# Optimization experiments

Measured on AMD Instinct MI355X. Metric: run time of the kernel, lower is better.

## Reference

```python
import jax, jax.numpy as jnp
import numpy as np
import math

IN_FEATURES = 8192
OUT_FEATURES = 8192
IN_MODES = (32, 16, 16)   # balanced power-of-two split of 8192 over order 3
OUT_MODES = (32, 16, 16)
RANKS = (1, 4, 4, 1)
TOKENS = 128


def setup_inputs() -> dict:
    key = jax.random.key(0)
    k_in, k0, k1, k2, kb = jax.random.split(key, 5)
    inputs = jax.random.normal(k_in, (TOKENS, IN_FEATURES), dtype=jnp.float32)
    # cores: (left_rank, out_mode, in_mode, right_rank), init N(0, 0.02)
    core0 = 0.02 * jax.random.normal(k0, (RANKS[0], OUT_MODES[0], IN_MODES[0], RANKS[1]), dtype=jnp.float32)
    core1 = 0.02 * jax.random.normal(k1, (RANKS[1], OUT_MODES[1], IN_MODES[1], RANKS[2]), dtype=jnp.float32)
    core2 = 0.02 * jax.random.normal(k2, (RANKS[2], OUT_MODES[2], IN_MODES[2], RANKS[3]), dtype=jnp.float32)
    bound = 1.0 / math.sqrt(IN_FEATURES)
    bias = jax.random.uniform(kb, (OUT_FEATURES,), minval=-bound, maxval=bound, dtype=jnp.float32)
    return {"inputs": inputs, "core0": core0, "core1": core1, "core2": core2, "bias": bias}


def _dense_weight(core0, core1, core2):
    # chain contraction over TT ranks
    t = jnp.tensordot(core0, core1, axes=([-1], [0]))  # (1, o0, i0, o1, i1, r2)
    t = jnp.tensordot(t, core2, axes=([-1], [0]))      # (1, o0, i0, o1, i1, o2, i2, 1)
    t = jnp.squeeze(t, axis=(0, -1))                    # (o0, i0, o1, i1, o2, i2)
    # out modes first, then in modes (matches torch permute [0,2,4,1,3,5])
    t = jnp.transpose(t, (0, 2, 4, 1, 3, 5))
    w = t.reshape(math.prod(OUT_MODES), math.prod(IN_MODES))
    return w[:OUT_FEATURES, :IN_FEATURES]


def reference(inputs, core0, core1, core2, bias):
    weight = _dense_weight(core0, core1, core2)  # [out, in]
    return inputs @ weight.T + bias
```

## Files before the change

kernel.cpp:

```cpp
#include <hip/hip_runtime.h>

__global__ __launch_bounds__(256, 4) void tt_k12(
    const float* __restrict__ x, const float* __restrict__ c1,
    const float* __restrict__ c2, const float* __restrict__ c0,
    float* __restrict__ y2, float* __restrict__ c0t)
{
    __shared__ float xs[64 * 20];
    __shared__ float c2s[64 * 20];
    __shared__ float y1s[64 * 68];
    const int tid = threadIdx.x;
    const int b = blockIdx.x;
    const int t = b >> 3, i0q = b & 7;

    if (b < 16) {
        int idx = (b << 8) | tid;
        c0t[idx] = c0[(idx & 31) * 128 + (idx >> 5)];
    }

    {
        float4 v = reinterpret_cast<const float4*>(x + t * 8192 + i0q * 1024)[tid];
        *reinterpret_cast<float4*>(&xs[(tid >> 2) * 20 + ((tid & 3) << 2)]) = v;
    }
#pragma unroll
    for (int m = 0; m < 4; ++m) {
        int q = (m << 8) | tid;
        float4 v = reinterpret_cast<const float4*>(c2)[q];
        *reinterpret_cast<float4*>(&c2s[(q >> 2) * 20 + ((q & 3) << 2)]) = v;
    }
    __syncthreads();

    {
        const int i0loc = tid >> 6;
        const int o2 = (tid >> 2) & 15;
        const int i1q = tid & 3;
        float cw[4][16];
#pragma unroll
        for (int r2 = 0; r2 < 4; ++r2)
#pragma unroll
            for (int m = 0; m < 4; ++m) {
                float4 v = *reinterpret_cast<const float4*>(
                    &c2s[((r2 << 4) | o2) * 20 + (m << 2)]);
                cw[r2][4*m+0] = v.x; cw[r2][4*m+1] = v.y;
                cw[r2][4*m+2] = v.z; cw[r2][4*m+3] = v.w;
            }
#pragma unroll
        for (int d = 0; d < 4; ++d) {
            int i1 = (i1q << 2) | d;
            float xv[16];
#pragma unroll
            for (int m = 0; m < 4; ++m) {
                float4 v = *reinterpret_cast<const float4*>(
                    &xs[((i0loc << 4) | i1) * 20 + (m << 2)]);
                xv[4*m+0] = v.x; xv[4*m+1] = v.y; xv[4*m+2] = v.z; xv[4*m+3] = v.w;
            }
            float s[4];
#pragma unroll
            for (int r2 = 0; r2 < 4; ++r2) {
                float a = 0.f;
#pragma unroll
                for (int i2 = 0; i2 < 16; ++i2) a += xv[i2] * cw[r2][i2];
                s[r2] = a;
            }
            *reinterpret_cast<float4*>(&y1s[((i0loc << 4) | o2) * 68 + (i1 << 2)]) =
                make_float4(s[0], s[1], s[2], s[3]);
        }
    }
    __syncthreads();

    const int lane = tid & 63;
    const int w = __builtin_amdgcn_readfirstlane(tid >> 6);
    float acc[16];
#pragma unroll
    for (int r = 0; r < 16; ++r) acc[r] = 0.f;
    const float* yrow = &y1s[lane * 68];
    const float4* c14 = reinterpret_cast<const float4*>(c1);
#pragma unroll 2
    for (int jq = 0; jq < 16; ++jq) {
        float4 yv = *reinterpret_cast<const float4*>(yrow + (jq << 2));
#pragma unroll
        for (int o1 = 0; o1 < 16; ++o1) {
            float4 cv = c14[(((w << 4) | o1) << 4) | jq];
            acc[o1] += yv.x*cv.x + yv.y*cv.y + yv.z*cv.z + yv.w*cv.w;
        }
    }
    const int k = (((i0q << 2) | (lane >> 4)) << 2) | w;
    float* outp = y2 + (((t << 7) | k) << 8) + (lane & 15);
#pragma unroll
    for (int o1 = 0; o1 < 16; ++o1) outp[o1 << 4] = acc[o1];
}

__global__ __launch_bounds__(256, 2) void tt_k3(
    const float* __restrict__ y2, const float* __restrict__ c0t,
    const float* __restrict__ bias, float* __restrict__ out)
{
    __shared__ float po[3][32][64];
    const int tid = threadIdx.x;
    const int lane = tid & 63;
    const int kh = __builtin_amdgcn_readfirstlane(tid >> 6);
    const int b = blockIdx.x;
    const int t = b >> 2;
    const int c = ((b & 3) << 6) | lane;
    float acc[32];
#pragma unroll
    for (int m = 0; m < 32; ++m) acc[m] = 0.f;
    const float* yp = y2 + (t << 15) + c;
    const float4* c04 = reinterpret_cast<const float4*>(c0t);
#pragma unroll 4
    for (int kk = 0; kk < 32; ++kk) {
        int k = (kh << 5) | kk;
        float v = yp[k << 8];
#pragma unroll
        for (int m = 0; m < 8; ++m) {
            float4 cv = c04[(k << 3) | m];
            acc[4*m+0] += cv.x * v;
            acc[4*m+1] += cv.y * v;
            acc[4*m+2] += cv.z * v;
            acc[4*m+3] += cv.w * v;
        }
    }
    if (kh != 0) {
#pragma unroll
        for (int m = 0; m < 32; ++m) po[kh-1][m][lane] = acc[m];
    }
    __syncthreads();
    if (kh == 0) {
#pragma unroll
        for (int m = 0; m < 32; ++m) {
            float s = acc[m] + po[0][m][lane] + po[1][m][lane] + po[2][m][lane]
                    + bias[(m << 8) | c];
            out[(t << 13) | (m << 8) | c] = s;
        }
    }
}

extern "C" void kernel_launch(void* const* d_in, const int* in_sizes, int n_in,
                              void* d_out, int out_size, void* d_ws, size_t ws_size,
                              hipStream_t stream) {
    const float* x    = (const float*)d_in[0];
    const float* c0   = (const float*)d_in[1];
    const float* c1   = (const float*)d_in[2];
    const float* c2   = (const float*)d_in[3];
    const float* bias = (const float*)d_in[4];
    float* out = (float*)d_out;

    float* y2  = (float*)d_ws;
    float* c0t = y2 + 4194304;

    tt_k12<<<1024, 256, 0, stream>>>(x, c1, c2, c0, y2, c0t);
    tt_k3 <<< 512, 256, 0, stream>>>(y2, c0t, bias, out);
}
```

Baseline: 96.25 us.

## Fuse all three TT core contractions into one kernel, keeping intermediates in LDS

Merges the two kernels into one, where each block handles one token and a quarter of the o2 outputs. It loads the whole token row into LDS and runs all three mode contractions there, so the 16 MB y2 intermediate never goes to global memory. Each block covers only 4 of the 16 o2 values, so it redoes the full first contraction input load, and the core0 and core1 stages read their cores from global memory or cache. It uses 64 KB of LDS per block, which lowers occupancy, and it removes the second launch and the c0 transpose.

Measured after the change: 111.2 us. 15.5% more time.

```diff
diff --git a/kernel.cpp b/kernel.cpp
--- a/kernel.cpp
+++ b/kernel.cpp
@@ -1,134 +1,121 @@
 #include <hip/hip_runtime.h>
 
-__global__ __launch_bounds__(256, 4) void tt_k12(
-    const float* __restrict__ x, const float* __restrict__ c1,
-    const float* __restrict__ c2, const float* __restrict__ c0,
-    float* __restrict__ y2, float* __restrict__ c0t)
+__global__ __launch_bounds__(256, 2) void tt_fused(
+    const float* __restrict__ x, const float* __restrict__ c0,
+    const float* __restrict__ c1, const float* __restrict__ c2,
+    const float* __restrict__ bias, float* __restrict__ out)
 {
-    __shared__ float xs[64 * 20];
-    __shared__ float c2s[64 * 20];
-    __shared__ float y1s[64 * 68];
+    __shared__ float smem[16384];
+    float* xs  = smem;
+    float* y1s = smem + 8192;
+    float* y2s = smem;
+
     const int tid = threadIdx.x;
-    const int b = blockIdx.x;
-    const int t = b >> 3, i0q = b & 7;
-
-    if (b < 16) {
-        int idx = (b << 8) | tid;
-        c0t[idx] = c0[(idx & 31) * 128 + (idx >> 5)];
-    }
+    const int b   = blockIdx.x;
+    const int t   = b >> 2, q = b & 3;
 
     {
-        float4 v = reinterpret_cast<const float4*>(x + t * 8192 + i0q * 1024)[tid];
-        *reinterpret_cast<float4*>(&xs[(tid >> 2) * 20 + ((tid & 3) << 2)]) = v;
-    }
+        const float4* xg = reinterpret_cast<const float4*>(x + t * 8192);
+        float4* xl = reinterpret_cast<float4*>(xs);
 #pragma unroll
-    for (int m = 0; m < 4; ++m) {
-        int q = (m << 8) | tid;
-        float4 v = reinterpret_cast<const float4*>(c2)[q];
-        *reinterpret_cast<float4*>(&c2s[(q >> 2) * 20 + ((q & 3) << 2)]) = v;
+        for (int m = 0; m < 8; ++m) xl[m * 256 + tid] = xg[m * 256 + tid];
     }
     __syncthreads();
 
     {
-        const int i0loc = tid >> 6;
-        const int o2 = (tid >> 2) & 15;
-        const int i1q = tid & 3;
-        float cw[4][16];
+        const int col = tid >> 1, i1h = tid & 1;
+        const int i0 = col >> 2, o2 = q * 4 + (col & 3);
+        float c2v[4][16];
 #pragma unroll
         for (int r2 = 0; r2 < 4; ++r2)
 #pragma unroll
             for (int m = 0; m < 4; ++m) {
-                float4 v = *reinterpret_cast<const float4*>(
-                    &c2s[((r2 << 4) | o2) * 20 + (m << 2)]);
-                cw[r2][4*m+0] = v.x; cw[r2][4*m+1] = v.y;
-                cw[r2][4*m+2] = v.z; cw[r2][4*m+3] = v.w;
+                float4 v = *reinterpret_cast<const float4*>(c2 + r2 * 256 + o2 * 16 + m * 4);
+                c2v[r2][4 * m + 0] = v.x; c2v[r2][4 * m + 1] = v.y;
+                c2v[r2][4 * m + 2] = v.z; c2v[r2][4 * m + 3] = v.w;
             }
 #pragma unroll
-        for (int d = 0; d < 4; ++d) {
-            int i1 = (i1q << 2) | d;
+        for (int ii = 0; ii < 8; ++ii) {
+            const int i1 = i1h * 8 + ii;
             float xv[16];
 #pragma unroll
             for (int m = 0; m < 4; ++m) {
-                float4 v = *reinterpret_cast<const float4*>(
-                    &xs[((i0loc << 4) | i1) * 20 + (m << 2)]);
-                xv[4*m+0] = v.x; xv[4*m+1] = v.y; xv[4*m+2] = v.z; xv[4*m+3] = v.w;
+                const int mp = (m + i0) & 3;
+                float4 v = *reinterpret_cast<const float4*>(xs + i0 * 256 + i1 * 16 + mp * 4);
+                xv[4 * mp + 0] = v.x; xv[4 * mp + 1] = v.y;
+                xv[4 * mp + 2] = v.z; xv[4 * mp + 3] = v.w;
             }
             float s[4];
 #pragma unroll
             for (int r2 = 0; r2 < 4; ++r2) {
                 float a = 0.f;
 #pragma unroll
-                for (int i2 = 0; i2 < 16; ++i2) a += xv[i2] * cw[r2][i2];
+                for (int i2 = 0; i2 < 16; ++i2) a += xv[i2] * c2v[r2][i2];
                 s[r2] = a;
             }
-            *reinterpret_cast<float4*>(&y1s[((i0loc << 4) | o2) * 68 + (i1 << 2)]) =
+            *reinterpret_cast<float4*>(y1s + (i1 * 128 + col) * 4) =
                 make_float4(s[0], s[1], s[2], s[3]);
         }
     }
     __syncthreads();
 
-    const int lane = tid & 63;
-    const int w = __builtin_amdgcn_readfirstlane(tid >> 6);
-    float acc[16];
+    {
+        const int lane = tid & 63;
+        const int r1 = __builtin_amdgcn_readfirstlane(tid >> 6);
+        float acc[16][2];
 #pragma unroll
-    for (int r = 0; r < 16; ++r) acc[r] = 0.f;
-    const float* yrow = &y1s[lane * 68];
-    const float4* c14 = reinterpret_cast<const float4*>(c1);
+        for (int rr = 0; rr < 16; ++rr) { acc[rr][0] = 0.f; acc[rr][1] = 0.f; }
 #pragma unroll 2
-    for (int jq = 0; jq < 16; ++jq) {
-        float4 yv = *reinterpret_cast<const float4*>(yrow + (jq << 2));
+        for (int jq = 0; jq < 16; ++jq) {
+            float4 yv0 = *reinterpret_cast<const float4*>(y1s + (jq * 128 + lane) * 4);
+            float4 yv1 = *reinterpret_cast<const float4*>(y1s + (jq * 128 + 64 + lane) * 4);
 #pragma unroll
-        for (int o1 = 0; o1 < 16; ++o1) {
-            float4 cv = c14[(((w << 4) | o1) << 4) | jq];
-            acc[o1] += yv.x*cv.x + yv.y*cv.y + yv.z*cv.z + yv.w*cv.w;
+            for (int rr = 0; rr < 16; ++rr) {
+                const int row = r1 * 16 + rr;
+                float4 cq = *reinterpret_cast<const float4*>(c1 + row * 64 + jq * 4);
+                acc[rr][0] += cq.x * yv0.x + cq.y * yv0.y + cq.z * yv0.z + cq.w * yv0.w;
+                acc[rr][1] += cq.x * yv1.x + cq.y * yv1.y + cq.z * yv1.z + cq.w * yv1.w;
+            }
+        }
+#pragma unroll
+        for (int g = 0; g < 2; ++g) {
+            const int col = g * 64 + lane;
+            const int i0 = col >> 2, o2l = col & 3;
+            const int k = i0 * 4 + r1;
+#pragma unroll
+            for (int rr = 0; rr < 16; ++rr)
+                y2s[k * 64 + (((rr + i0) & 15) << 2) + o2l] = acc[rr][g];
         }
     }
-    const int k = (((i0q << 2) | (lane >> 4)) << 2) | w;
-    float* outp = y2 + (((t << 7) | k) << 8) + (lane & 15);
+    __syncthreads();
+
+    {
+        const int cd  = tid & 63;
+        const int o0g = __builtin_amdgcn_readfirstlane(tid >> 6);
+        const int o1 = cd >> 2, o2l = cd & 3;
+        float acc[8];
 #pragma unroll
-    for (int o1 = 0; o1 < 16; ++o1) outp[o1 << 4] = acc[o1];
-}
-
-__global__ __launch_bounds__(256, 2) void tt_k3(
-    const float* __restrict__ y2, const float* __restrict__ c0t,
-    const float* __restrict__ bias, float* __restrict__ out)
-{
-    __shared__ float po[3][32][64];
-    const int tid = threadIdx.x;
-    const int lane = tid & 63;
-    const int kh = __builtin_amdgcn_readfirstlane(tid >> 6);
-    const int b = blockIdx.x;
-    const int t = b >> 2;
-    const int c = ((b & 3) << 6) | lane;
-    float acc[32];
+        for (int m = 0; m < 8; ++m) acc[m] = 0.f;
+#pragma unroll 4
+        for (int kq = 0; kq < 32; ++kq) {
+            float yv[4];
 #pragma unroll
-    for (int m = 0; m < 32; ++m) acc[m] = 0.f;
-    const float* yp = y2 + (t << 15) + c;
-    const float4* c04 = reinterpret_cast<const float4*>(c0t);
-#pragma unroll 4
-    for (int kk = 0; kk < 32; ++kk) {
-        int k = (kh << 5) | kk;
-        float v = yp[k << 8];
+            for (int dk = 0; dk < 4; ++dk) {
+                const int k = kq * 4 + dk;
+                yv[dk] = y2s[k * 64 + (((o1 + (k >> 2)) & 15) << 2) + o2l];
+            }
+#pragma unroll
+            for (int m = 0; m < 8; ++m) {
+                const int o0 = o0g * 8 + m;
+                float4 cq = *reinterpret_cast<const float4*>(c0 + o0 * 128 + kq * 4);
+                acc[m] += cq.x * yv[0] + cq.y * yv[1] + cq.z * yv[2] + cq.w * yv[3];
+            }
+        }
 #pragma unroll
         for (int m = 0; m < 8; ++m) {
-            float4 cv = c04[(k << 3) | m];
-            acc[4*m+0] += cv.x * v;
-            acc[4*m+1] += cv.y * v;
-            acc[4*m+2] += cv.z * v;
-            acc[4*m+3] += cv.w * v;
-        }
-    }
-    if (kh != 0) {
-#pragma unroll
-        for (int m = 0; m < 32; ++m) po[kh-1][m][lane] = acc[m];
-    }
-    __syncthreads();
-    if (kh == 0) {
-#pragma unroll
-        for (int m = 0; m < 32; ++m) {
-            float s = acc[m] + po[0][m][lane] + po[1][m][lane] + po[2][m][lane]
-                    + bias[(m << 8) | c];
-            out[(t << 13) | (m << 8) | c] = s;
+            const int o0 = o0g * 8 + m;
+            const int o = o0 * 256 + o1 * 16 + q * 4 + o2l;
+            out[t * 8192 + o] = acc[m] + bias[o];
         }
     }
 }
@@ -142,10 +129,7 @@
     const float* c2   = (const float*)d_in[3];
     const float* bias = (const float*)d_in[4];
     float* out = (float*)d_out;
+    (void)d_ws; (void)ws_size;
 
-    float* y2  = (float*)d_ws;
-    float* c0t = y2 + 4194304;
-
-    tt_k12<<<1024, 256, 0, stream>>>(x, c1, c2, c0, y2, c0t);
-    tt_k3 <<< 512, 256, 0, stream>>>(y2, c0t, bias, out);
+    tt_fused<<<512, 256, 0, stream>>>(x, c0, c1, c2, bias, out);
 }
```
